# Kernel optimization log

Measured on AMD Instinct MI355X. Metric: run time of the kernel, lower is better.

Reference implementation:

```python
import jax, jax.numpy as jnp
import numpy as np

N_STEPS = 8  # fixed-step Dormand-Prince RK45 steps replacing adaptive dopri5


def setup_inputs() -> dict:
    key = jax.random.key(0)
    ks = jax.random.split(key, 12)
    B, I, H = 16384, 128, 256
    s_ih = 1.0 / np.sqrt(I)
    s_hh = 1.0 / np.sqrt(H)
    return {
        "inputs": jax.random.normal(ks[0], (B, I), jnp.float32),
        "h0": jax.random.normal(ks[1], (B, H), jnp.float32),
        "c0": jax.random.normal(ks[2], (B, H), jnp.float32),
        "ts": jax.random.uniform(ks[3], (B,), jnp.float32),  # per-example end times in [0,1)
        "W_ih": jax.random.normal(ks[4], (4 * H, I), jnp.float32) * s_ih,
        "W_hh": jax.random.normal(ks[5], (4 * H, H), jnp.float32) * s_hh,
        "b_ih": jax.random.normal(ks[6], (4 * H,), jnp.float32) * s_hh,
        "b_hh": jax.random.normal(ks[7], (4 * H,), jnp.float32) * s_hh,
        "W1": jax.random.normal(ks[8], (H, H), jnp.float32) * s_hh,
        "b1": jax.random.normal(ks[9], (H,), jnp.float32) * s_hh,
        "W2": jax.random.normal(ks[10], (H, H), jnp.float32) * s_hh,
        "b2": jax.random.normal(ks[11], (H,), jnp.float32) * s_hh,
    }


def reference(inputs, h0, c0, ts, W_ih, W_hh, b_ih, b_hh, W1, b1, W2, b2):
    # ODE vector field: fc = Linear -> Tanh -> Linear (autonomous)
    def f(h):
        return jnp.tanh(h @ W1.T + b1) @ W2.T + b2

    dt = (ts / N_STEPS)[:, None]  # [B,1] per-example step size

    def rk45_step(h, _):
        k1 = f(h)
        k2 = f(h + dt * (0.2 * k1))
        k3 = f(h + dt * (3.0 / 40.0 * k1 + 9.0 / 40.0 * k2))
        k4 = f(h + dt * (44.0 / 45.0 * k1 - 56.0 / 15.0 * k2 + 32.0 / 9.0 * k3))
        k5 = f(h + dt * (19372.0 / 6561.0 * k1 - 25360.0 / 2187.0 * k2
                         + 64448.0 / 6561.0 * k3 - 212.0 / 729.0 * k4))
        k6 = f(h + dt * (9017.0 / 3168.0 * k1 - 355.0 / 33.0 * k2
                         + 46732.0 / 5247.0 * k3 + 49.0 / 176.0 * k4
                         - 5103.0 / 18656.0 * k5))
        h_new = h + dt * (35.0 / 384.0 * k1 + 500.0 / 1113.0 * k3
                          + 125.0 / 192.0 * k4 - 2187.0 / 6784.0 * k5
                          + 11.0 / 84.0 * k6)
        return h_new, None

    h_ode, _ = jax.lax.scan(rk45_step, h0, None, length=N_STEPS)

    def lstm_cell(x, h, c):
        gates = x @ W_ih.T + b_ih + h @ W_hh.T + b_hh  # [B,4H]
        i, fg, g, o = jnp.split(gates, 4, axis=-1)
        i = jax.nn.sigmoid(i)
        fg = jax.nn.sigmoid(fg)
        g = jnp.tanh(g)
        o = jax.nn.sigmoid(o)
        c_new = fg * c + i * g
        return o * jnp.tanh(c_new), c_new

    # two (weight-shared) LSTMCell applications as in the original forward
    h1, c1 = lstm_cell(inputs, h_ode, c0)
    h2, c2 = lstm_cell(inputs, h1, c1)
    return h2, c2
```

## Files before the change

### kernel.cpp

```cpp
#include <hip/hip_runtime.h>

#define B_TOT 16384
#define HD 256
#define ID 128
#define BT 32
#define NSTEP 8
#define YP 264
#define XP 136

typedef float    f32x4  __attribute__((ext_vector_type(4)));
typedef float    f32x16 __attribute__((ext_vector_type(16)));
typedef _Float16 f16x8  __attribute__((ext_vector_type(8)));
typedef _Float16 f16x4  __attribute__((ext_vector_type(4)));
typedef _Float16 f16x2  __attribute__((ext_vector_type(2)));

__device__ __forceinline__ float fast_rcp(float x){ return __builtin_amdgcn_rcpf(x); }
__device__ __forceinline__ float fast_exp2(float x){ return __builtin_amdgcn_exp2f(x); }
__device__ __forceinline__ float fast_tanh(float x){
  return 1.0f - 2.0f*fast_rcp(1.0f + fast_exp2(x*2.8853900817779268f));
}
__device__ __forceinline__ float fast_sigmoid(float x){
  return fast_rcp(1.0f + fast_exp2(x*-1.4426950408889634f));
}

__global__ void cvt_f32_f16(const float* __restrict__ src, _Float16* __restrict__ dst, int n4){
  int i = blockIdx.x*256 + threadIdx.x;
  if (i < n4){
    float4 v = ((const float4*)src)[i];
    f16x4 t = {(_Float16)v.x, (_Float16)v.y, (_Float16)v.z, (_Float16)v.w};
    *(f16x4*)(dst + (size_t)i*4) = t;
  }
}

#define KP(i) ((float)kpk[i][pk][hw])

__global__ __launch_bounds__(512, 2)
void ode_lstm(const float* __restrict__ inputs, const float* __restrict__ h0,
              const float* __restrict__ c0,     const float* __restrict__ ts,
              const float* __restrict__ b_ih,   const float* __restrict__ b_hh,
              const float* __restrict__ b1,     const float* __restrict__ b2,
              const _Float16* __restrict__ W1h, const _Float16* __restrict__ W2h,
              const _Float16* __restrict__ Wihh,const _Float16* __restrict__ Whhh,
              float* __restrict__ out)
{
  __shared__ __align__(16) _Float16 yl[BT*YP];
  __shared__ __align__(16) _Float16 ul[BT*YP];
  __shared__ __align__(16) _Float16 xl[BT*XP];
  __shared__ __align__(16) float b1l[HD], b2l[HD], bsl[4*HD];
  __shared__ float dtl[BT];

  const int tid  = threadIdx.x;
  const int wv   = tid >> 6;
  const int lane = tid & 63;
  const int l31  = lane & 31;
  const int hh   = lane >> 5;
  const int row0 = blockIdx.x * BT;
  const int cb   = wv*32 + hh*4;
  const int yrow = l31*YP + cb;

  #pragma unroll
  for (int it = 0; it < 2; ++it){
    int idx = tid + it*512;
    int r = idx >> 5, c4 = idx & 31;
    float4 v = ((const float4*)inputs)[(size_t)(row0 + r)*(ID/4) + c4];
    f16x4 t = {(_Float16)v.x, (_Float16)v.y, (_Float16)v.z, (_Float16)v.w};
    *(f16x4*)(xl + r*XP + c4*4) = t;
  }
  if (tid < HD){ b1l[tid] = b1[tid]; b2l[tid] = b2[tid]; }
  bsl[tid]       = b_ih[tid]       + b_hh[tid];
  bsl[tid + 512] = b_ih[tid + 512] + b_hh[tid + 512];
  if (tid < BT) dtl[tid] = ts[row0 + tid] * (1.0f/NSTEP);

  f16x8 W1f[16], W2f[16];
  {
    const _Float16* w1p = W1h + (size_t)(wv*32 + l31)*HD + hh*8;
    const _Float16* w2p = W2h + (size_t)(wv*32 + l31)*HD + hh*8;
    #pragma unroll
    for (int kt = 0; kt < 16; ++kt){
      W1f[kt] = *(const f16x8*)(w1p + kt*16);
      W2f[kt] = *(const f16x8*)(w2p + kt*16);
    }
  }

  f32x4 h4[4];
  #pragma unroll
  for (int g2 = 0; g2 < 4; ++g2){
    f32x4 hv = *(const f32x4*)(h0 + (size_t)(row0 + l31)*HD + cb + 8*g2);
    h4[g2] = hv;
    f16x4 t = {(_Float16)hv[0], (_Float16)hv[1], (_Float16)hv[2], (_Float16)hv[3]};
    *(f16x4*)(yl + yrow + 8*g2) = t;
  }
  __syncthreads();
  const float dtv = dtl[l31];

  auto gemm16 = [&](const f16x8 (&Wf)[16], const _Float16* __restrict__ act)->f32x16{
    f32x16 a = {};
    const _Float16* bp = act + l31*YP + hh*8;
    #pragma unroll
    for (int kt = 0; kt < 16; ++kt){
      f16x8 Bf = *(const f16x8*)(bp + kt*16);
      a = __builtin_amdgcn_mfma_f32_32x32x16_f16(Wf[kt], Bf, a, 0, 0, 0);
    }
    return a;
  };

  auto phase1 = [&](){
    f32x16 a = gemm16(W1f, yl);
    #pragma unroll
    for (int g2 = 0; g2 < 4; ++g2){
      f32x4 bv = *(const f32x4*)(b1l + cb + 8*g2);
      f16x4 uv;
      #pragma unroll
      for (int r3 = 0; r3 < 4; ++r3)
        uv[r3] = (_Float16)fast_tanh(a[g2*4 + r3] + bv[r3]);
      *(f16x4*)(ul + yrow + 8*g2) = uv;
    }
    __syncthreads();
  };

  #define STAGE(SIDX, YEXPR)                                              \
    phase1();                                                             \
    { f32x16 a2 = gemm16(W2f, ul);                                        \
      _Pragma("unroll")                                                   \
      for (int g2 = 0; g2 < 4; ++g2){                                     \
        f32x4 bv = *(const f32x4*)(b2l + cb + 8*g2);                      \
        f16x4 yv;                                                         \
        _Pragma("unroll")                                                 \
        for (int r3 = 0; r3 < 4; ++r3){                                   \
          const int r = g2*4 + r3; const int pk = r>>1; const int hw = r&1;\
          float kd = dtv*(a2[r] + bv[r3]);                                \
          if (SIDX < 5) kpk[SIDX][pk][hw] = (_Float16)kd;                 \
          yv[r3] = (_Float16)(YEXPR);                                     \
        }                                                                 \
        *(f16x4*)(yl + yrow + 8*g2) = yv;                                 \
      }                                                                   \
    }                                                                     \
    __syncthreads();

  #pragma unroll 1
  for (int step = 0; step < NSTEP; ++step){
    f16x2 kpk[5][8];

    STAGE(0, h4[g2][r3] + 0.2f*kd)
    STAGE(1, h4[g2][r3] + 0.075f*KP(0) + 0.225f*kd)
    STAGE(2, h4[g2][r3] + (44.0f/45.0f)*KP(0) + (-56.0f/15.0f)*KP(1)
                        + (32.0f/9.0f)*kd)
    STAGE(3, h4[g2][r3] + (19372.0f/6561.0f)*KP(0) + (-25360.0f/2187.0f)*KP(1)
                        + (64448.0f/6561.0f)*KP(2) + (-212.0f/729.0f)*kd)
    STAGE(4, h4[g2][r3] + (9017.0f/3168.0f)*KP(0) + (-355.0f/33.0f)*KP(1)
                        + (46732.0f/5247.0f)*KP(2) + (49.0f/176.0f)*KP(3)
                        + (-5103.0f/18656.0f)*kd)
    phase1();
    { f32x16 a2 = gemm16(W2f, ul);
      #pragma unroll
      for (int g2 = 0; g2 < 4; ++g2){
        f32x4 bv = *(const f32x4*)(b2l + cb + 8*g2);
        f16x4 yv;
        #pragma unroll
        for (int r3 = 0; r3 < 4; ++r3){
          const int r = g2*4 + r3; const int pk = r>>1; const int hw = r&1;
          float kd = dtv*(a2[r] + bv[r3]);
          float hn = h4[g2][r3] + (35.0f/384.0f)*KP(0) + (500.0f/1113.0f)*KP(2)
                   + (125.0f/192.0f)*KP(3) + (-2187.0f/6784.0f)*KP(4)
                   + (11.0f/84.0f)*kd;
          h4[g2][r3] = hn;
          yv[r3] = (_Float16)hn;
        }
        *(f16x4*)(yl + yrow + 8*g2) = yv;
      }
    }
    __syncthreads();
  }

  f32x16 agx[4] = {};
  {
    const _Float16* bp = xl + l31*XP + hh*8;
    #pragma unroll 2
    for (int kt = 0; kt < 8; ++kt){
      f16x8 Bf = *(const f16x8*)(bp + kt*16);
      #pragma unroll
      for (int g = 0; g < 4; ++g){
        f16x8 Af = *(const f16x8*)(Wihh + (size_t)(g*HD + wv*32 + l31)*ID + kt*16 + hh*8);
        agx[g] = __builtin_amdgcn_mfma_f32_32x32x16_f16(Af, Bf, agx[g], 0, 0, 0);
      }
    }
  }
  f32x4 c4[4];
  #pragma unroll
  for (int g2 = 0; g2 < 4; ++g2)
    c4[g2] = *(const f32x4*)(c0 + (size_t)(row0 + l31)*HD + cb + 8*g2);

  #pragma unroll 1
  for (int cell = 0; cell < 2; ++cell){
    f32x16 ag[4];
    #pragma unroll
    for (int g = 0; g < 4; ++g) ag[g] = agx[g];
    const _Float16* hsrc = (cell == 0) ? yl : ul;
    const _Float16* bp = hsrc + l31*YP + hh*8;
    #pragma unroll 2
    for (int kt = 0; kt < 16; ++kt){
      f16x8 Bf = *(const f16x8*)(bp + kt*16);
      #pragma unroll
      for (int g = 0; g < 4; ++g){
        f16x8 Af = *(const f16x8*)(Whhh + (size_t)(g*HD + wv*32 + l31)*HD + kt*16 + hh*8);
        ag[g] = __builtin_amdgcn_mfma_f32_32x32x16_f16(Af, Bf, ag[g], 0, 0, 0);
      }
    }
    #pragma unroll
    for (int g2 = 0; g2 < 4; ++g2){
      f32x4 bi = *(const f32x4*)(bsl + 0*HD + cb + 8*g2);
      f32x4 bf = *(const f32x4*)(bsl + 1*HD + cb + 8*g2);
      f32x4 bg = *(const f32x4*)(bsl + 2*HD + cb + 8*g2);
      f32x4 bo = *(const f32x4*)(bsl + 3*HD + cb + 8*g2);
      f16x4 hv; f32x4 ho, co;
      #pragma unroll
      for (int r3 = 0; r3 < 4; ++r3){
        const int r = g2*4 + r3;
        float iv = fast_sigmoid(ag[0][r] + bi[r3]);
        float fv = fast_sigmoid(ag[1][r] + bf[r3]);
        float gv = fast_tanh   (ag[2][r] + bg[r3]);
        float ov = fast_sigmoid(ag[3][r] + bo[r3]);
        float cn = fv*c4[g2][r3] + iv*gv;
        c4[g2][r3] = cn;
        float hn = ov*fast_tanh(cn);
        hv[r3] = (_Float16)hn; ho[r3] = hn; co[r3] = cn;
      }
      if (cell == 0){
        *(f16x4*)(ul + yrow + 8*g2) = hv;
      } else {
        size_t o = (size_t)(row0 + l31)*HD + cb + 8*g2;
        *(f32x4*)(out + o) = ho;
        *(f32x4*)(out + (size_t)B_TOT*HD + o) = co;
      }
    }
    if (cell == 0) __syncthreads();
  }
}

extern "C" void kernel_launch(void* const* d_in, const int* in_sizes, int n_in,
                              void* d_out, int out_size, void* d_ws, size_t ws_size,
                              hipStream_t stream) {
  (void)in_sizes; (void)n_in; (void)out_size; (void)ws_size;
  const float* inputs = (const float*)d_in[0];
  const float* h0     = (const float*)d_in[1];
  const float* c0     = (const float*)d_in[2];
  const float* ts     = (const float*)d_in[3];
  const float* W_ih   = (const float*)d_in[4];
  const float* W_hh   = (const float*)d_in[5];
  const float* b_ih   = (const float*)d_in[6];
  const float* b_hh   = (const float*)d_in[7];
  const float* W1     = (const float*)d_in[8];
  const float* b1     = (const float*)d_in[9];
  const float* W2     = (const float*)d_in[10];
  const float* b2     = (const float*)d_in[11];
  float* out = (float*)d_out;

  _Float16* wsh  = (_Float16*)d_ws;
  _Float16* W1h  = wsh;
  _Float16* W2h  = wsh + 65536;
  _Float16* Wihh = wsh + 131072;
  _Float16* Whhh = wsh + 262144;

  cvt_f32_f16<<<64,  256, 0, stream>>>(W1,   W1h,  16384);
  cvt_f32_f16<<<64,  256, 0, stream>>>(W2,   W2h,  16384);
  cvt_f32_f16<<<128, 256, 0, stream>>>(W_ih, Wihh, 32768);
  cvt_f32_f16<<<256, 256, 0, stream>>>(W_hh, Whhh, 65536);

  ode_lstm<<<B_TOT/BT, 512, 0, stream>>>(inputs, h0, c0, ts, b_ih, b_hh, b1, b2,
                                         W1h, W2h, Wihh, Whhh, out);
}
```

Before: 415.4 us.

## Merge weight-conversion launches, convert W1/W2 in-kernel, split MFMA accumulators

Replaces four fp16 conversion launches with one combined launch for W_ih/W_hh. W1/W2 are now read as fp32 and converted to fp16 in registers inside the main kernel, and the b1/b2 biases move from shared memory into fp16 registers. The ODE GEMM uses two interleaved accumulators to break the MFMA dependency chain. The input-weight GEMM is now recomputed inside each LSTM cell iteration, trading extra MFMA work for fewer live accumulator registers. The fp16 bias storage slightly lowers precision and adds register pressure.

```diff
diff --git a/kernel.cpp b/kernel.cpp
--- a/kernel.cpp
+++ b/kernel.cpp
@@ -23,13 +23,16 @@
   return fast_rcp(1.0f + fast_exp2(x*-1.4426950408889634f));
 }
 
-__global__ void cvt_f32_f16(const float* __restrict__ src, _Float16* __restrict__ dst, int n4){
+__global__ void cvt_wts(const float* __restrict__ s0, const float* __restrict__ s1,
+                        _Float16* __restrict__ d0, _Float16* __restrict__ d1,
+                        int n0, int n1){
   int i = blockIdx.x*256 + threadIdx.x;
-  if (i < n4){
-    float4 v = ((const float4*)src)[i];
-    f16x4 t = {(_Float16)v.x, (_Float16)v.y, (_Float16)v.z, (_Float16)v.w};
-    *(f16x4*)(dst + (size_t)i*4) = t;
-  }
+  const float* s; _Float16* d; int j;
+  if (i < n0){ s = s0; d = d0; j = i; }
+  else       { s = s1; d = d1; j = i - n0; if (j >= n1) return; }
+  float4 v = ((const float4*)s)[j];
+  f16x4 t = {(_Float16)v.x, (_Float16)v.y, (_Float16)v.z, (_Float16)v.w};
+  *(f16x4*)(d + (size_t)j*4) = t;
 }
 
 #define KP(i) ((float)kpk[i][pk][hw])
@@ -39,14 +42,14 @@
               const float* __restrict__ c0,     const float* __restrict__ ts,
               const float* __restrict__ b_ih,   const float* __restrict__ b_hh,
               const float* __restrict__ b1,     const float* __restrict__ b2,
-              const _Float16* __restrict__ W1h, const _Float16* __restrict__ W2h,
+              const float* __restrict__ W1,     const float* __restrict__ W2,
               const _Float16* __restrict__ Wihh,const _Float16* __restrict__ Whhh,
               float* __restrict__ out)
 {
   __shared__ __align__(16) _Float16 yl[BT*YP];
   __shared__ __align__(16) _Float16 ul[BT*YP];
   __shared__ __align__(16) _Float16 xl[BT*XP];
-  __shared__ __align__(16) float b1l[HD], b2l[HD], bsl[4*HD];
+  __shared__ __align__(16) float bsl[4*HD];
   __shared__ float dtl[BT];
 
   const int tid  = threadIdx.x;
@@ -66,19 +69,36 @@
     f16x4 t = {(_Float16)v.x, (_Float16)v.y, (_Float16)v.z, (_Float16)v.w};
     *(f16x4*)(xl + r*XP + c4*4) = t;
   }
-  if (tid < HD){ b1l[tid] = b1[tid]; b2l[tid] = b2[tid]; }
   bsl[tid]       = b_ih[tid]       + b_hh[tid];
   bsl[tid + 512] = b_ih[tid + 512] + b_hh[tid + 512];
   if (tid < BT) dtl[tid] = ts[row0 + tid] * (1.0f/NSTEP);
 
+  f16x4 b1p[4], b2p[4];
+  #pragma unroll
+  for (int g2 = 0; g2 < 4; ++g2){
+    f32x4 t1 = *(const f32x4*)(b1 + cb + 8*g2);
+    f32x4 t2 = *(const f32x4*)(b2 + cb + 8*g2);
+    #pragma unroll
+    for (int r3 = 0; r3 < 4; ++r3){ b1p[g2][r3] = (_Float16)t1[r3]; b2p[g2][r3] = (_Float16)t2[r3]; }
+  }
+
   f16x8 W1f[16], W2f[16];
   {
-    const _Float16* w1p = W1h + (size_t)(wv*32 + l31)*HD + hh*8;
-    const _Float16* w2p = W2h + (size_t)(wv*32 + l31)*HD + hh*8;
+    const float* w1p = W1 + (size_t)(wv*32 + l31)*HD + hh*8;
+    const float* w2p = W2 + (size_t)(wv*32 + l31)*HD + hh*8;
     #pragma unroll
     for (int kt = 0; kt < 16; ++kt){
-      W1f[kt] = *(const f16x8*)(w1p + kt*16);
-      W2f[kt] = *(const f16x8*)(w2p + kt*16);
+      f32x4 a = *(const f32x4*)(w1p + kt*16);
+      f32x4 b = *(const f32x4*)(w1p + kt*16 + 4);
+      f32x4 c = *(const f32x4*)(w2p + kt*16);
+      f32x4 d = *(const f32x4*)(w2p + kt*16 + 4);
+      f16x8 w1, w2;
+      #pragma unroll
+      for (int j = 0; j < 4; ++j){
+        w1[j] = (_Float16)a[j]; w1[4+j] = (_Float16)b[j];
+        w2[j] = (_Float16)c[j]; w2[4+j] = (_Float16)d[j];
+      }
+      W1f[kt] = w1; W2f[kt] = w2;
     }
   }
 
@@ -94,25 +114,26 @@
   const float dtv = dtl[l31];
 
   auto gemm16 = [&](const f16x8 (&Wf)[16], const _Float16* __restrict__ act)->f32x16{
-    f32x16 a = {};
+    f32x16 a0 = {}, a1 = {};
     const _Float16* bp = act + l31*YP + hh*8;
     #pragma unroll
-    for (int kt = 0; kt < 16; ++kt){
-      f16x8 Bf = *(const f16x8*)(bp + kt*16);
-      a = __builtin_amdgcn_mfma_f32_32x32x16_f16(Wf[kt], Bf, a, 0, 0, 0);
-    }
-    return a;
+    for (int kt = 0; kt < 16; kt += 2){
+      f16x8 B0 = *(const f16x8*)(bp + kt*16);
+      f16x8 B1 = *(const f16x8*)(bp + kt*16 + 16);
+      a0 = __builtin_amdgcn_mfma_f32_32x32x16_f16(Wf[kt],   B0, a0, 0, 0, 0);
+      a1 = __builtin_amdgcn_mfma_f32_32x32x16_f16(Wf[kt+1], B1, a1, 0, 0, 0);
+    }
+    return a0 + a1;
   };
 
   auto phase1 = [&](){
     f32x16 a = gemm16(W1f, yl);
     #pragma unroll
     for (int g2 = 0; g2 < 4; ++g2){
-      f32x4 bv = *(const f32x4*)(b1l + cb + 8*g2);
       f16x4 uv;
       #pragma unroll
       for (int r3 = 0; r3 < 4; ++r3)
-        uv[r3] = (_Float16)fast_tanh(a[g2*4 + r3] + bv[r3]);
+        uv[r3] = (_Float16)fast_tanh(a[g2*4 + r3] + (float)b1p[g2][r3]);
       *(f16x4*)(ul + yrow + 8*g2) = uv;
     }
     __syncthreads();
@@ -123,12 +144,11 @@
     { f32x16 a2 = gemm16(W2f, ul);                                        \
       _Pragma("unroll")                                                   \
       for (int g2 = 0; g2 < 4; ++g2){                                     \
-        f32x4 bv = *(const f32x4*)(b2l + cb + 8*g2);                      \
         f16x4 yv;                                                         \
         _Pragma("unroll")                                                 \
         for (int r3 = 0; r3 < 4; ++r3){                                   \
           const int r = g2*4 + r3; const int pk = r>>1; const int hw = r&1;\
-          float kd = dtv*(a2[r] + bv[r3]);                                \
+          float kd = dtv*(a2[r] + (float)b2p[g2][r3]);                    \
           if (SIDX < 5) kpk[SIDX][pk][hw] = (_Float16)kd;                 \
           yv[r3] = (_Float16)(YEXPR);                                     \
         }                                                                 \
@@ -154,12 +174,11 @@
     { f32x16 a2 = gemm16(W2f, ul);
       #pragma unroll
       for (int g2 = 0; g2 < 4; ++g2){
-        f32x4 bv = *(const f32x4*)(b2l + cb + 8*g2);
         f16x4 yv;
         #pragma unroll
         for (int r3 = 0; r3 < 4; ++r3){
           const int r = g2*4 + r3; const int pk = r>>1; const int hw = r&1;
-          float kd = dtv*(a2[r] + bv[r3]);
+          float kd = dtv*(a2[r] + (float)b2p[g2][r3]);
           float hn = h4[g2][r3] + (35.0f/384.0f)*KP(0) + (500.0f/1113.0f)*KP(2)
                    + (125.0f/192.0f)*KP(3) + (-2187.0f/6784.0f)*KP(4)
                    + (11.0f/84.0f)*kd;
@@ -172,19 +191,6 @@
     __syncthreads();
   }
 
-  f32x16 agx[4] = {};
-  {
-    const _Float16* bp = xl + l31*XP + hh*8;
-    #pragma unroll 2
-    for (int kt = 0; kt < 8; ++kt){
-      f16x8 Bf = *(const f16x8*)(bp + kt*16);
-      #pragma unroll
-      for (int g = 0; g < 4; ++g){
-        f16x8 Af = *(const f16x8*)(Wihh + (size_t)(g*HD + wv*32 + l31)*ID + kt*16 + hh*8);
-        agx[g] = __builtin_amdgcn_mfma_f32_32x32x16_f16(Af, Bf, agx[g], 0, 0, 0);
-      }
-    }
-  }
   f32x4 c4[4];
   #pragma unroll
   for (int g2 = 0; g2 < 4; ++g2)
@@ -192,18 +198,30 @@
 
   #pragma unroll 1
   for (int cell = 0; cell < 2; ++cell){
-    f32x16 ag[4];
-    #pragma unroll
-    for (int g = 0; g < 4; ++g) ag[g] = agx[g];
-    const _Float16* hsrc = (cell == 0) ? yl : ul;
-    const _Float16* bp = hsrc + l31*YP + hh*8;
-    #pragma unroll 2
-    for (int kt = 0; kt < 16; ++kt){
-      f16x8 Bf = *(const f16x8*)(bp + kt*16);
-      #pragma unroll
-      for (int g = 0; g < 4; ++g){
-        f16x8 Af = *(const f16x8*)(Whhh + (size_t)(g*HD + wv*32 + l31)*HD + kt*16 + hh*8);
-        ag[g] = __builtin_amdgcn_mfma_f32_32x32x16_f16(Af, Bf, ag[g], 0, 0, 0);
+    f32x16 ag[4] = {};
+    {
+      const _Float16* bp = xl + l31*XP + hh*8;
+      #pragma unroll 4
+      for (int kt = 0; kt < 8; ++kt){
+        f16x8 Bf = *(const f16x8*)(bp + kt*16);
+        #pragma unroll
+        for (int g = 0; g < 4; ++g){
+          f16x8 Af = *(const f16x8*)(Wihh + (size_t)(g*HD + wv*32 + l31)*ID + kt*16 + hh*8);
+          ag[g] = __builtin_amdgcn_mfma_f32_32x32x16_f16(Af, Bf, ag[g], 0, 0, 0);
+        }
+      }
+    }
+    {
+      const _Float16* hsrc = (cell == 0) ? yl : ul;
+      const _Float16* bp = hsrc + l31*YP + hh*8;
+      #pragma unroll 4
+      for (int kt = 0; kt < 16; ++kt){
+        f16x8 Bf = *(const f16x8*)(bp + kt*16);
+        #pragma unroll
+        for (int g = 0; g < 4; ++g){
+          f16x8 Af = *(const f16x8*)(Whhh + (size_t)(g*HD + wv*32 + l31)*HD + kt*16 + hh*8);
+          ag[g] = __builtin_amdgcn_mfma_f32_32x32x16_f16(Af, Bf, ag[g], 0, 0, 0);
+        }
       }
     }
     #pragma unroll
@@ -256,16 +274,11 @@
   float* out = (float*)d_out;
 
   _Float16* wsh  = (_Float16*)d_ws;
-  _Float16* W1h  = wsh;
-  _Float16* W2h  = wsh + 65536;
-  _Float16* Wihh = wsh + 131072;
-  _Float16* Whhh = wsh + 262144;
-
-  cvt_f32_f16<<<64,  256, 0, stream>>>(W1,   W1h,  16384);
-  cvt_f32_f16<<<64,  256, 0, stream>>>(W2,   W2h,  16384);
-  cvt_f32_f16<<<128, 256, 0, stream>>>(W_ih, Wihh, 32768);
-  cvt_f32_f16<<<256, 256, 0, stream>>>(W_hh, Whhh, 65536);
+  _Float16* Wihh = wsh;
+  _Float16* Whhh = wsh + 131072;
+
+  cvt_wts<<<384, 256, 0, stream>>>(W_ih, W_hh, Wihh, Whhh, 32768, 65536);
 
   ode_lstm<<<B_TOT/BT, 512, 0, stream>>>(inputs, h0, c0, ts, b_ih, b_hh, b1, b2,
-                                         W1h, W2h, Wihh, Whhh, out);
-}
+                                         W1, W2, Wihh, Whhh, out);
+}
```

Result: slower. 737.3 us (+77.5%).
